# Performance work log

Hardware: AMD Instinct MI355X
Metric: run time of the kernel (lower is better)

The kernel has to match this reference:

```python
import jax, jax.numpy as jnp
import numpy as np

EPS = 1e-5
NEG_SLOPE = 0.01  # F.leaky_relu default


def setup_inputs() -> dict:
    key = jax.random.key(0)
    k1, k2, k3, k4 = jax.random.split(key, 4)
    b, c, n, p = 4, 32, 2048, 12
    out_size = 32
    n_agg, n_scal = 7, 3
    X = jax.random.normal(k1, (b, c, n, p), dtype=jnp.float32)
    A = jax.random.uniform(k2, (n, n), dtype=jnp.float32)  # dense weighted adjacency
    fan = n_agg * n_scal * c
    Theta = jax.random.normal(k3, (fan, out_size), dtype=jnp.float32) * np.float32(np.sqrt(2.0 / (fan + out_size)))
    stdv = np.float32(1.0 / np.sqrt(out_size))
    Bias = jax.random.uniform(k4, (out_size,), dtype=jnp.float32, minval=-stdv, maxval=stdv)
    return {"X": X, "A": A, "Theta": Theta, "Bias": Bias}


def _aggregate(Xp, A):
    # Xp: [b, p, n, c], A: [n, n]. One fused pass: all aggregators share A@(.) reductions.
    deg = jnp.sum(A, axis=1)                   # [n]
    d = jnp.maximum(deg, EPS)[:, None]         # [n, 1]
    agg = lambda M: jnp.einsum('nm,bpmc->bpnc', A, M)
    m1 = agg(Xp) / d                           # E[x_j]
    m2 = agg(Xp * Xp) / d                      # E[x_j^2]
    m3 = agg(Xp ** 3) / d                      # E[x_j^3]
    m4 = agg(Xp ** 4) / d                      # E[x_j^4]
    e_pos = jnp.exp(Xp)
    e_neg = jnp.exp(-Xp)
    softmax = agg(Xp * e_pos) / (agg(e_pos) + EPS)
    softmin = agg(Xp * e_neg) / (agg(e_neg) + EPS)
    var = jax.nn.relu(m2 - m1 * m1)
    std = jnp.sqrt(var + EPS)
    # distance: E_j[(x_i - x_j)^2] expanded via moments (no [n,n,c] intermediate)
    dist = Xp * Xp - 2.0 * Xp * m1 + m2
    # second moment of squared distance: E_j[(x_i - x_j)^4]
    ed2 = Xp ** 4 - 4.0 * Xp ** 3 * m1 + 6.0 * Xp ** 2 * m2 - 4.0 * Xp * m3 + m4
    d_std = jnp.sqrt(jax.nn.relu(ed2 - dist * dist) + EPS)
    # order matches aggregators list: softmin, softmax, normalized_mean, std, var, distance, d_std
    return jnp.concatenate([softmin, softmax, m1, std, var, dist, d_std], axis=-1)


def reference(X, A, Theta, Bias):
    # X: [b, c, n, p] -> [b, p, n, c]
    Xp = jnp.transpose(X, (0, 3, 2, 1))
    out = _aggregate(Xp, A)                    # [b, p, n, 7c]
    deg = jnp.sum(A, axis=1)
    logd = jnp.log(deg + 1.0)
    delta = jnp.mean(logd)                     # avg log-degree (PNA scaler normalizer)
    s = (logd / delta)[None, None, :, None]
    # scalers: identity, amplification, attenuation
    out = jnp.concatenate([out, out * s, out / jnp.maximum(s, EPS)], axis=-1)  # [b, p, n, 21c]
    out = jnp.einsum('bpnc,co->bpno', out, Theta) + Bias
    out = jnp.transpose(out, (0, 3, 2, 1))     # [b, o, n, p]
    # dropout is identity at inference (training=False)
    return jax.nn.leaky_relu(out, NEG_SLOPE)
```

## Files before the change

kernel.cpp:

```cpp
#include <hip/hip_runtime.h>
#include <hip/hip_bf16.h>
#include <cstdint>
#include <cstddef>

typedef unsigned short u16;
typedef __bf16 bf16x8 __attribute__((ext_vector_type(8)));
typedef float f32x4 __attribute__((ext_vector_type(4)));
typedef unsigned int u32x4 __attribute__((ext_vector_type(4)));

#define EPSF 1e-5f

__device__ __forceinline__ float b2f(u16 u) {
  unsigned int i = ((unsigned int)u) << 16;
  return __builtin_bit_cast(float, i);
}
__device__ __forceinline__ u16 f2b(float f) {
  unsigned int u = __builtin_bit_cast(unsigned int, f);
  u = u + 0x7fffu + ((u >> 16) & 1u);
  return (u16)(u >> 16);
}

__device__ __forceinline__ void async_load16(const u16* g, u16* l) {
  __builtin_amdgcn_global_load_lds(
      (__attribute__((address_space(1))) void*)(g),
      (__attribute__((address_space(3))) void*)(l), 16, 0, 0);
}

__global__ __launch_bounds__(256) void prep_kernel(
    const void* __restrict__ X, const void* __restrict__ A,
    const void* __restrict__ Th, u16* __restrict__ Abf, u16* __restrict__ Ft,
    float* __restrict__ deg, float* __restrict__ logd, u16* __restrict__ ThT) {
  __shared__ int sbad;
  __shared__ float Xl[256 * 13];
  __shared__ float red[4];
  const int tid = threadIdx.x;
  if (tid == 0) sbad = 0;
  __syncthreads();
  {
    const u16* Xu = (const u16*)X;
    int bad = 0;
#pragma unroll
    for (int q = 0; q < 8; ++q) {
      float a = fabsf(b2f(Xu[q * 256 + tid]));
      if (!(a <= 1e4f)) bad = 1;
    }
    if (bad) atomicOr(&sbad, 1);
  }
  __syncthreads();
  const int isf32 = sbad;
  const int bid = blockIdx.x;

  if (bid < 2048) {
    const int row = bid;
    float s = 0.f;
    uint4 st;
    if (isf32) {
      const float4* Af = (const float4*)A + (size_t)row * 512 + tid * 2;
      float4 a = Af[0], b = Af[1];
      s = a.x + a.y + a.z + a.w + b.x + b.y + b.z + b.w;
      u16 o[8] = {f2b(a.x), f2b(a.y), f2b(a.z), f2b(a.w),
                  f2b(b.x), f2b(b.y), f2b(b.z), f2b(b.w)};
      st = *(const uint4*)o;
    } else {
      st = ((const uint4*)A)[(size_t)row * 256 + tid];
      const u16* o = (const u16*)&st;
#pragma unroll
      for (int k = 0; k < 8; ++k) s += b2f(o[k]);
    }
    *(uint4*)(Abf + (size_t)row * 2048 + tid * 8) = st;
#pragma unroll
    for (int off = 32; off > 0; off >>= 1) s += __shfl_down(s, off, 64);
    const int lane = tid & 63, w = tid >> 6;
    if (lane == 0) red[w] = s;
    __syncthreads();
    if (tid == 0) {
      float t = red[0] + red[1] + red[2] + red[3];
      deg[row] = t;
      logd[row] = logf(t + 1.f);
    }
  } else if (bid < 3072) {
    const int blk = bid - 2048;
    const int mc = blk & 7;
    const int ch = (blk >> 3) & 31;
    const int b  = blk >> 8;
    const size_t g0 = ((size_t)(b * 32 + ch) * 2048 + (size_t)mc * 256) * 12;
    if (isf32) {
      const float4* Xg = (const float4*)((const float*)X + g0);
#pragma unroll
      for (int q = 0; q < 3; ++q) {
        const int id = q * 256 + tid;
        const float4 v = Xg[id];
        const int j = id * 4, row = j / 12, col = j % 12;
        Xl[row * 13 + col]     = v.x;
        Xl[row * 13 + col + 1] = v.y;
        Xl[row * 13 + col + 2] = v.z;
        Xl[row * 13 + col + 3] = v.w;
      }
    } else {
      const u16* Xg = (const u16*)X + g0;
#pragma unroll
      for (int q = 0; q < 12; ++q) {
        const int id = q * 256 + tid;
        Xl[(id / 12) * 13 + id % 12] = b2f(Xg[id]);
      }
    }
    __syncthreads();
    const int m = tid;
    const int gm = mc * 256 + m;
#pragma unroll
    for (int p = 0; p < 12; ++p) {
      const float x = Xl[m * 13 + p];
      const float x2 = x * x, x3 = x2 * x, x4 = x2 * x2;
      const float e = __expf(x), en = __expf(-x);
      const float vals[8] = {x, x2, x3, x4, x * e, e, x * en, en};
      const size_t cb = (size_t)(b * 12 + p) * 256 + ch;
#pragma unroll
      for (int f = 0; f < 8; ++f)
        Ft[(cb + (size_t)f * 32) * 2048 + gm] = f2b(vals[f]);
    }
  } else {
    const int e = (bid - 3072) * 256 + tid;
    if (e < 21504) {
      const int k = e >> 5, o = e & 31;
      ThT[o * 672 + k] = isf32 ? f2b(((const float*)Th)[e]) : ((const u16*)Th)[e];
    }
  }
}

__global__ __launch_bounds__(256) void gemm_kernel(const u16* __restrict__ A,
                                                   const u16* __restrict__ Ft,
                                                   u16* __restrict__ Y) {
  __shared__ __attribute__((aligned(16))) u16 smem[2 * 128 * 64];
  u16* As = smem;
  u16* Bs = smem + 128 * 64;
  const int tid = threadIdx.x;
  const int wave = tid >> 6;
  const int lane = tid & 63;
  const int l15 = lane & 15;
  const int quad = lane >> 4;
  const int wm = wave >> 1;
  const int wn = wave & 1;

  const int i4 = blockIdx.x;
  const int xcd = i4 & 7;
  const int s4 = i4 >> 3;
  const int bm = (xcd >> 1) * 4 + (s4 & 3);
  const int bn = (xcd & 1) * 48 + (s4 >> 2);

  const int lrow = lane >> 3;
  const int schunk = (lane & 7) ^ lrow;
  const u16* gA = A  + (size_t)(bm * 128 + wave * 32 + lrow) * 2048 + schunk * 8;
  const u16* gB = Ft + (size_t)(bn * 128 + wave * 32 + lrow) * 2048 + schunk * 8;
  u16* lA = As + wave * 32 * 64 + lane * 8;
  u16* lB = Bs + wave * 32 * 64 + lane * 8;

  f32x4 acc[4][4];
#pragma unroll
  for (int i = 0; i < 4; ++i)
#pragma unroll
    for (int j = 0; j < 4; ++j) acc[i][j] = (f32x4){0.f, 0.f, 0.f, 0.f};

  for (int kk = 0; kk < 2048; kk += 64) {
    __syncthreads();
#pragma unroll
    for (int i = 0; i < 4; ++i) {
      async_load16(gA + (size_t)i * (8 * 2048) + kk, lA + i * (8 * 64));
      async_load16(gB + (size_t)i * (8 * 2048) + kk, lB + i * (8 * 64));
    }
    __syncthreads();
#pragma unroll
    for (int ks = 0; ks < 2; ++ks) {
      const int ca = ((ks * 4 + quad) ^ (l15 & 7)) * 8;
      bf16x8 af[4], bfr[4];
#pragma unroll
      for (int t = 0; t < 4; ++t)
        af[t] = *(const bf16x8*)(As + (wm * 64 + t * 16 + l15) * 64 + ca);
#pragma unroll
      for (int t = 0; t < 4; ++t)
        bfr[t] = *(const bf16x8*)(Bs + (wn * 64 + t * 16 + l15) * 64 + ca);
#pragma unroll
      for (int mt = 0; mt < 4; ++mt)
#pragma unroll
        for (int nt = 0; nt < 4; ++nt)
          acc[mt][nt] = __builtin_amdgcn_mfma_f32_16x16x32_bf16(af[mt], bfr[nt],
                                                                acc[mt][nt], 0, 0, 0);
    }
  }

  __syncthreads();
  u16* Cs = smem;
#pragma unroll
  for (int mt = 0; mt < 4; ++mt)
#pragma unroll
    for (int nt = 0; nt < 4; ++nt) {
      const int row = wm * 64 + mt * 16 + quad * 4;
      const int col = wn * 64 + nt * 16 + l15;
#pragma unroll
      for (int j = 0; j < 4; ++j)
        Cs[(row + j) * 128 + col] = f2b(acc[mt][nt][j]);
    }
  __syncthreads();
  const size_t ybase = (size_t)(bm * 128) * 12288 + (size_t)bn * 128;
#pragma unroll
  for (int q = 0; q < 8; ++q) {
    const int id = q * 256 + tid;
    const int r = id >> 4, c = (id & 15) * 8;
    __builtin_nontemporal_store(*(const u32x4*)(Cs + r * 128 + c),
                                (u32x4*)(Y + ybase + (size_t)r * 12288 + c));
  }
}

__global__ __launch_bounds__(256) void epilogue_kernel(
    const u16* __restrict__ Y, const u16* __restrict__ Fx,
    const float* __restrict__ deg, const float* __restrict__ logd,
    const u16* __restrict__ ThT, const void* __restrict__ Bias,
    void* __restrict__ out, const u16* __restrict__ Xu) {
  __shared__ __attribute__((aligned(16))) u16 Ys[32 * 264];
  __shared__ u16 Xs[32 * 33];
  __shared__ __attribute__((aligned(16))) u16 feats[32 * 680];
  __shared__ int sbad;
  __shared__ float red[4];
  const int tid = threadIdx.x;
  if (tid == 0) sbad = 0;
  __syncthreads();
  float ls = 0.f;
  {
    int bad = 0;
#pragma unroll
    for (int q = 0; q < 8; ++q) {
      float a = fabsf(b2f(Xu[q * 256 + tid]));
      if (!(a <= 1e4f)) bad = 1;
      ls += logd[q * 256 + tid];
    }
    if (bad) atomicOr(&sbad, 1);
  }
#pragma unroll
  for (int off = 32; off > 0; off >>= 1) ls += __shfl_down(ls, off, 64);
  if ((tid & 63) == 0) red[tid >> 6] = ls;
  __syncthreads();
  const int isf32 = sbad;
  const float delta = (red[0] + red[1] + red[2] + red[3]) * (1.0f / 2048.0f);

  const int nc = blockIdx.x;
  const int b  = blockIdx.y;
  const int pz = blockIdx.z;

  const int nl = tid >> 3;
  const int chg = tid & 7;
  const int inode = nc * 32 + nl;
  const float d = fmaxf(deg[inode], EPSF);
  const float rd = 1.0f / d;
  const float s = logd[inode] / delta;
  const float is = 1.0f / fmaxf(s, EPSF);

  const int wave = tid >> 6, lane = tid & 63;
  const int l15 = lane & 15, quad = lane >> 4;
  const int mt = wave >> 1, nt = wave & 1;
  const int o = nt * 16 + l15;
  const float bias = isf32 ? ((const float*)Bias)[o] : b2f(((const u16*)Bias)[o]);

  float r[4][6];

#pragma unroll
  for (int pp = 0; pp < 6; ++pp) {
    const int p = pz * 6 + pp;
    const int bp = b * 12 + p;
    __syncthreads();
#pragma unroll
    for (int q = 0; q < 4; ++q) {
      const int id = q * 256 + tid;
      const int rr = id >> 5, ck = id & 31;
      *(u32x4*)(Ys + rr * 264 + ck * 8) = __builtin_nontemporal_load(
          (const u32x4*)(Y + (size_t)(nc * 32 + rr) * 12288 + (size_t)bp * 256 + ck * 8));
      Xs[rr * 33 + ck] = Fx[(size_t)(bp * 256 + rr) * 2048 + nc * 32 + ck];
    }
    __syncthreads();

    const u16* yr = Ys + nl * 264;
#pragma unroll
    for (int cc = 0; cc < 4; ++cc) {
      const int ch = chg * 4 + cc;
      const float m1 = b2f(yr[ch]) * rd;
      const float m2 = b2f(yr[32 + ch]) * rd;
      const float m3 = b2f(yr[64 + ch]) * rd;
      const float m4 = b2f(yr[96 + ch]) * rd;
      const float smx = b2f(yr[128 + ch]) / (b2f(yr[160 + ch]) + EPSF);
      const float smn = b2f(yr[192 + ch]) / (b2f(yr[224 + ch]) + EPSF);
      const float x = b2f(Xs[ch * 33 + nl]);
      const float var = fmaxf(m2 - m1 * m1, 0.f);
      const float stdv = sqrtf(var + EPSF);
      const float x2 = x * x, x3 = x2 * x, x4 = x2 * x2;
      const float dist = x2 - 2.f * x * m1 + m2;
      const float ed2 = x4 - 4.f * x3 * m1 + 6.f * x2 * m2 - 4.f * x * m3 + m4;
      const float dstd = sqrtf(fmaxf(ed2 - dist * dist, 0.f) + EPSF);
      const float f7[7] = {smn, smx, m1, stdv, var, dist, dstd};
#pragma unroll
      for (int a = 0; a < 7; ++a) {
        const int k = a * 32 + ch;
        feats[nl * 680 + k]       = f2b(f7[a]);
        feats[nl * 680 + 224 + k] = f2b(f7[a] * s);
        feats[nl * 680 + 448 + k] = f2b(f7[a] * is);
      }
    }
    __syncthreads();

    f32x4 acc = (f32x4){0.f, 0.f, 0.f, 0.f};
#pragma unroll
    for (int kt = 0; kt < 21; ++kt) {
      bf16x8 a  = *(const bf16x8*)(feats + (mt * 16 + l15) * 680 + kt * 32 + quad * 8);
      bf16x8 bb = *(const bf16x8*)(ThT + (size_t)o * 672 + kt * 32 + quad * 8);
      acc = __builtin_amdgcn_mfma_f32_16x16x32_bf16(a, bb, acc, 0, 0, 0);
    }
#pragma unroll
    for (int j = 0; j < 4; ++j) r[j][pp] = acc[j];
  }

#pragma unroll
  for (int j = 0; j < 4; ++j) {
    const int node = mt * 16 + quad * 4 + j;
    const int ig = nc * 32 + node;
    const size_t oi = ((size_t)(b * 32 + o) * 2048 + ig) * 12 + pz * 6;
    float v[6];
#pragma unroll
    for (int k = 0; k < 6; ++k) {
      float t = r[j][k] + bias;
      v[k] = t > 0.f ? t : 0.01f * t;
    }
    if (isf32) {
      float* dst = (float*)out + oi;
      *(float2*)(dst)     = (float2){v[0], v[1]};
      *(float2*)(dst + 2) = (float2){v[2], v[3]};
      *(float2*)(dst + 4) = (float2){v[4], v[5]};
    } else {
      u16* dst = (u16*)out + oi;
#pragma unroll
      for (int k = 0; k < 6; ++k) dst[k] = f2b(v[k]);
    }
  }
}

extern "C" void kernel_launch(void* const* d_in, const int* in_sizes, int n_in,
                              void* d_out, int out_size, void* d_ws, size_t ws_size,
                              hipStream_t stream) {
  const void* X    = d_in[0];
  const void* A    = d_in[1];
  const void* Th   = d_in[2];
  const void* Bias = d_in[3];
  char* ws = (char*)d_ws;

  u16*   Ft   = (u16*)(ws);
  u16*   Y    = (u16*)(ws + 50331648);
  u16*   Abf  = (u16*)(ws + 100663296);
  float* deg  = (float*)(ws + 109051904);
  float* logd = (float*)(ws + 109060096);
  u16*   ThT  = (u16*)(ws + 109068288);

  prep_kernel<<<3156, 256, 0, stream>>>(X, A, Th, Abf, Ft, deg, logd, ThT);
  gemm_kernel<<<1536, 256, 0, stream>>>(Abf, Ft, Y);
  epilogue_kernel<<<dim3(64, 4, 2), 256, 0, stream>>>(Y, Ft, deg, logd, ThT,
                                                      Bias, d_out, (const u16*)X);
}
```

Baseline: 214.9 us.

## Vectorize feature stores and prefetch next plane's aggregates into registers

The feature-prep kernel now has each thread handle 8 consecutive nodes for one plane and write 16-byte vectorized stores of the bf16 features, replacing scalar 2-byte stores. The epilogue kernel prefetches the next plane's Y and X tiles into registers while computing the current plane, overlapping global loads with compute. It also packs the LDS feature writes into 8-byte stores. In exchange, the prep loop uses only 384 work items over 256 threads, so some threads idle in the second pass, and the prefetch raises register use.

```diff
diff --git a/kernel.cpp b/kernel.cpp
--- a/kernel.cpp
+++ b/kernel.cpp
@@ -4,6 +4,7 @@
 #include <cstddef>
 
 typedef unsigned short u16;
+typedef unsigned long long u64;
 typedef __bf16 bf16x8 __attribute__((ext_vector_type(8)));
 typedef float f32x4 __attribute__((ext_vector_type(4)));
 typedef unsigned int u32x4 __attribute__((ext_vector_type(4)));
@@ -105,18 +106,38 @@
       }
     }
     __syncthreads();
-    const int m = tid;
-    const int gm = mc * 256 + m;
-#pragma unroll
-    for (int p = 0; p < 12; ++p) {
-      const float x = Xl[m * 13 + p];
-      const float x2 = x * x, x3 = x2 * x, x4 = x2 * x2;
-      const float e = __expf(x), en = __expf(-x);
-      const float vals[8] = {x, x2, x3, x4, x * e, e, x * en, en};
+    for (int u = tid; u < 384; u += 256) {
+      const int p = u >> 5;
+      const int mg = u & 31;
+      float x[8], e[8], en[8];
+#pragma unroll
+      for (int j = 0; j < 8; ++j) {
+        x[j] = Xl[(mg * 8 + j) * 13 + p];
+        e[j] = __expf(x[j]);
+        en[j] = __expf(-x[j]);
+      }
       const size_t cb = (size_t)(b * 12 + p) * 256 + ch;
-#pragma unroll
-      for (int f = 0; f < 8; ++f)
-        Ft[(cb + (size_t)f * 32) * 2048 + gm] = f2b(vals[f]);
+      const int gmb = mc * 256 + mg * 8;
+#pragma unroll
+      for (int f = 0; f < 8; ++f) {
+        u16 o[8];
+#pragma unroll
+        for (int j = 0; j < 8; ++j) {
+          const float xx = x[j];
+          const float x2 = xx * xx;
+          float v;
+          if      (f == 0) v = xx;
+          else if (f == 1) v = x2;
+          else if (f == 2) v = x2 * xx;
+          else if (f == 3) v = x2 * x2;
+          else if (f == 4) v = xx * e[j];
+          else if (f == 5) v = e[j];
+          else if (f == 6) v = xx * en[j];
+          else             v = en[j];
+          o[j] = f2b(v);
+        }
+        *(uint4*)(Ft + (cb + (size_t)f * 32) * 2048 + gmb) = *(const uint4*)o;
+      }
     }
   } else {
     const int e = (bid - 3072) * 256 + tid;
@@ -259,24 +280,47 @@
   const int o = nt * 16 + l15;
   const float bias = isf32 ? ((const float*)Bias)[o] : b2f(((const u16*)Bias)[o]);
 
+  const int srr = tid >> 5 ? 0 : 0;
   float r[4][6];
-
-#pragma unroll
-  for (int pp = 0; pp < 6; ++pp) {
-    const int p = pz * 6 + pp;
-    const int bp = b * 12 + p;
-    __syncthreads();
+  u32x4 yreg[4];
+  u16 xreg[4];
+  {
+    const int bp0 = b * 12 + pz * 6;
 #pragma unroll
     for (int q = 0; q < 4; ++q) {
       const int id = q * 256 + tid;
       const int rr = id >> 5, ck = id & 31;
-      *(u32x4*)(Ys + rr * 264 + ck * 8) = __builtin_nontemporal_load(
-          (const u32x4*)(Y + (size_t)(nc * 32 + rr) * 12288 + (size_t)bp * 256 + ck * 8));
-      Xs[rr * 33 + ck] = Fx[(size_t)(bp * 256 + rr) * 2048 + nc * 32 + ck];
-    }
-    __syncthreads();
+      yreg[q] = __builtin_nontemporal_load(
+          (const u32x4*)(Y + (size_t)(nc * 32 + rr) * 12288 + (size_t)bp0 * 256 + ck * 8));
+      xreg[q] = Fx[(size_t)(bp0 * 256 + rr) * 2048 + nc * 32 + ck];
+    }
+  }
+
+#pragma unroll
+  for (int pp = 0; pp < 6; ++pp) {
+    __syncthreads();
+#pragma unroll
+    for (int q = 0; q < 4; ++q) {
+      const int id = q * 256 + tid;
+      const int rr = id >> 5, ck = id & 31;
+      *(u32x4*)(Ys + rr * 264 + ck * 8) = yreg[q];
+      Xs[rr * 33 + ck] = xreg[q];
+    }
+    __syncthreads();
+    if (pp < 5) {
+      const int bpn = b * 12 + pz * 6 + pp + 1;
+#pragma unroll
+      for (int q = 0; q < 4; ++q) {
+        const int id = q * 256 + tid;
+        const int rr = id >> 5, ck = id & 31;
+        yreg[q] = __builtin_nontemporal_load(
+            (const u32x4*)(Y + (size_t)(nc * 32 + rr) * 12288 + (size_t)bpn * 256 + ck * 8));
+        xreg[q] = Fx[(size_t)(bpn * 256 + rr) * 2048 + nc * 32 + ck];
+      }
+    }
 
     const u16* yr = Ys + nl * 264;
+    float fv[7][4];
 #pragma unroll
     for (int cc = 0; cc < 4; ++cc) {
       const int ch = chg * 4 + cc;
@@ -293,14 +337,23 @@
       const float dist = x2 - 2.f * x * m1 + m2;
       const float ed2 = x4 - 4.f * x3 * m1 + 6.f * x2 * m2 - 4.f * x * m3 + m4;
       const float dstd = sqrtf(fmaxf(ed2 - dist * dist, 0.f) + EPSF);
-      const float f7[7] = {smn, smx, m1, stdv, var, dist, dstd};
-#pragma unroll
-      for (int a = 0; a < 7; ++a) {
-        const int k = a * 32 + ch;
-        feats[nl * 680 + k]       = f2b(f7[a]);
-        feats[nl * 680 + 224 + k] = f2b(f7[a] * s);
-        feats[nl * 680 + 448 + k] = f2b(f7[a] * is);
-      }
+      fv[0][cc] = smn; fv[1][cc] = smx; fv[2][cc] = m1; fv[3][cc] = stdv;
+      fv[4][cc] = var; fv[5][cc] = dist; fv[6][cc] = dstd;
+    }
+#pragma unroll
+    for (int a = 0; a < 7; ++a) {
+      u16 o0[4], o1[4], o2[4];
+#pragma unroll
+      for (int cc = 0; cc < 4; ++cc) {
+        const float t = fv[a][cc];
+        o0[cc] = f2b(t);
+        o1[cc] = f2b(t * s);
+        o2[cc] = f2b(t * is);
+      }
+      const int base = nl * 680 + a * 32 + chg * 4;
+      *(u64*)(feats + base)       = *(const u64*)o0;
+      *(u64*)(feats + base + 224) = *(const u64*)o1;
+      *(u64*)(feats + base + 448) = *(const u64*)o2;
     }
     __syncthreads();
 
```

Result: no change. 219.0 us (+1.9%).
